# Kernel tuning notes

Measured on AMD Instinct MI355X. Metric: run time of the kernel, lower is better.

Reference implementation:

```python
import jax, jax.numpy as jnp
import numpy as np

RADIUS = 8
NUM = 200
EPS = 1e-8


def _conv2d(x, k, pad_mode):
    # x: [B,1,H,W], k: [kh,kw]; same-size conv with given numpy-style padding mode
    ph, pw = k.shape[0] // 2, k.shape[1] // 2
    xp = jnp.pad(x, ((0, 0), (0, 0), (ph, ph), (pw, pw)), mode=pad_mode)
    return jax.lax.conv_general_dilated(
        xp, k[None, None], (1, 1), 'VALID',
        dimension_numbers=('NCHW', 'OIHW', 'NCHW'))


def _gauss_kernel7():
    xs = np.arange(7, dtype=np.float32) - 3.0
    g = np.exp(-0.5 * xs ** 2)
    g /= g.sum()
    return jnp.asarray(np.outer(g, g))


def get_corners(imgs):
    B, _, H, W = imgs.shape
    # kornia rgb_to_grayscale
    gray = 0.299 * imgs[:, 0:1] + 0.587 * imgs[:, 1:2] + 0.114 * imgs[:, 2:3]
    # kornia CornerGFTT: sobel gradients (normalized), gaussian-smoothed structure tensor, min eigenvalue
    sob = jnp.array([[-1., 0., 1.], [-2., 0., 2.], [-1., 0., 1.]], jnp.float32) / 8.0
    dx = _conv2d(gray, sob, 'edge')
    dy = _conv2d(gray, sob.T, 'edge')
    g = _gauss_kernel7()
    dx2 = _conv2d(dx * dx, g, 'reflect')
    dy2 = _conv2d(dy * dy, g, 'reflect')
    dxy = _conv2d(dx * dy, g, 'reflect')
    tr = dx2 + dy2
    det = dx2 * dy2 - dxy * dxy
    resp = 0.5 * (tr - jnp.sqrt(jnp.abs(tr * tr - 4.0 * det)))  # GFTT score (min eigval)
    # kornia nms2d with 5x5 window: keep local maxima
    mp = jax.lax.reduce_window(resp, -jnp.inf, jax.lax.max,
                               (1, 1, 5, 5), (1, 1, 1, 1),
                               [(0, 0), (0, 0), (2, 2), (2, 2)])
    resp = jnp.where(resp == mp, resp, 0.0)
    # unfold/mask/fold with kernel=stride=RADIUS == per non-overlapping 8x8 block:
    # keep elements equal to the block max and > 0
    r = RADIUS
    blk = resp.reshape(B, 1, H // r, r, W // r, r)
    bmax = blk.max(axis=(3, 5), keepdims=True)
    blk = jnp.where((blk > 0) & (blk == bmax), blk, 0.0)
    corners = blk.reshape(B, H * W)
    # top-200 scatter then binarize
    vals, idx = jax.lax.top_k(corners, NUM)
    out = jnp.zeros_like(corners).at[jnp.arange(B)[:, None], idx].set(vals)
    return (out > 0).astype(imgs.dtype).reshape(B, 1, H, W)


def setup_inputs() -> dict:
    key = jax.random.key(0)
    k1, k2, k3, k4 = jax.random.split(key, 4)
    B, N, D, H, W = 16, 2048, 256, 384, 384
    return {
        'descriptors': jax.random.normal(k1, (B, N, D), jnp.float32),
        'scores': jax.random.uniform(k2, (B, N), jnp.float32),
        'scores_dense': jax.random.normal(k3, (B, 1, H, W), jnp.float32),
        'imgs': jax.random.uniform(k4, (B, 3, H, W), jnp.float32),
    }


def reference(descriptors, scores, scores_dense, imgs):
    corners = get_corners(imgs)
    # all-pairs cosine similarity within each batch: pcos[b,i,j]
    norms = jnp.linalg.norm(descriptors, axis=-1)  # [B,N]
    dots = jnp.einsum('bnd,bmd->bnm', descriptors, descriptors)
    pcos = dots / jnp.maximum(norms[:, :, None] * norms[:, None, :], EPS)
    # BCEWithLogitsLoss(scores_dense, corners), mean reduction
    bce = jnp.mean(jnp.logaddexp(0.0, scores_dense) - scores_dense * corners)
    return bce + jnp.mean(jax.nn.relu(pcos))
```

## Files before the change

kernel.cpp:

```cpp
#include <hip/hip_runtime.h>

#define H 384
#define W 384
#define HWSZ (H * W)
#define NB 16
#define ND 2048
#define DD 256

#define OFF_RESP  256
#define OFF_CVAL  9437440
#define OFF_CPOS  9584896
#define OFF_DESCB 9732352
#define OFF_INV   26509568
#define OFF_PSOFT 26640640
#define OFF_PGEMM 26643200
#define OFF_PCORN 26652160

__device__ __forceinline__ int clampi(int v) { return v < 0 ? 0 : (v > 383 ? 383 : v); }
__device__ __forceinline__ int refl(int v) { return v < 0 ? -v : (v >= 384 ? 766 - v : v); }

__device__ __forceinline__ unsigned f2e4m3(float x) {
  float a = fabsf(x);
  unsigned s = (__float_as_uint(x) >> 31) << 7;
  if (a >= 448.f) return s | 0x7E;
  if (a < 0.015625f) {
    int m = (int)rintf(a * 512.f);
    return s | (unsigned)m;
  }
  unsigned u = __float_as_uint(a);
  u += 0x7FFFF + ((u >> 20) & 1);
  unsigned e = (u >> 23) - 120;
  unsigned m = (u >> 20) & 7;
  return s | (e << 3) | m;
}

typedef float f32x4 __attribute__((ext_vector_type(4)));

__device__ __forceinline__ void load_lds16(const void* g, void* l) {
  __builtin_amdgcn_global_load_lds((const __attribute__((address_space(1))) void*)g,
                                   (__attribute__((address_space(3))) void*)l, 16, 0, 0);
}

__global__ __launch_bounds__(256) void stage1_kernel(const float* __restrict__ imgs,
                                                     float* __restrict__ resp,
                                                     const float* __restrict__ desc,
                                                     unsigned char* __restrict__ descF8,
                                                     float* __restrict__ invn,
                                                     const float4* __restrict__ sd4,
                                                     float* __restrict__ psoft) {
  __shared__ float gl[40][41];
  __shared__ float p0[38][39], p1[38][39], p2[38][39];
  __shared__ float t0[38][33], t1[38][33], t2[38][33];
  __shared__ float r4s[4];

  if (blockIdx.x >= 10496) {
    int sb = blockIdx.x - 10496;
    float s = 0.f;
    int base = sb * 256 + threadIdx.x;
#pragma unroll
    for (int it = 0; it < 4; it++) {
      float4 v = sd4[base + it * 147456];
      s += fmaxf(v.x, 0.f) + log1pf(expf(-fabsf(v.x))) +
           fmaxf(v.y, 0.f) + log1pf(expf(-fabsf(v.y))) +
           fmaxf(v.z, 0.f) + log1pf(expf(-fabsf(v.z))) +
           fmaxf(v.w, 0.f) + log1pf(expf(-fabsf(v.w)));
    }
    for (int off = 32; off; off >>= 1) s += __shfl_down(s, off, 64);
    if ((threadIdx.x & 63) == 0) r4s[threadIdx.x >> 6] = s;
    __syncthreads();
    if (threadIdx.x == 0) psoft[sb] = r4s[0] + r4s[1] + r4s[2] + r4s[3];
    return;
  }

  if (blockIdx.x >= 2304) {
    int wave = threadIdx.x >> 6, lane = threadIdx.x & 63;
    int row = (blockIdx.x - 2304) * 4 + wave;
    const float4* src = (const float4*)(desc + (size_t)row * DD);
    float4 v = src[lane];
    unsigned pk = f2e4m3(v.x) | (f2e4m3(v.y) << 8) | (f2e4m3(v.z) << 16) | (f2e4m3(v.w) << 24);
    ((unsigned*)(descF8 + (size_t)row * DD))[lane] = pk;
    float ss = v.x * v.x + v.y * v.y + v.z * v.z + v.w * v.w;
    for (int off = 32; off; off >>= 1) ss += __shfl_down(ss, off, 64);
    if (lane == 0) invn[row] = 1.f / fmaxf(sqrtf(ss), 1e-4f);
    return;
  }

  const float GW[7] = {0.0044330482f, 0.0540055826f, 0.2420362294f, 0.3990502160f,
                       0.2420362294f, 0.0540055826f, 0.0044330482f};
  int bid = blockIdx.x;
  int b = bid / 144;
  int t = bid % 144;
  int Y0 = (t / 12) * 32, X0 = (t % 12) * 32;
  const float* ib = imgs + (size_t)b * 3 * HWSZ;

  for (int i = threadIdx.x; i < 1600; i += 256) {
    int r = i / 40, c = i % 40;
    int gy = clampi(Y0 - 4 + r), gx = clampi(X0 - 4 + c);
    const float* p = ib + gy * W + gx;
    gl[r][c] = 0.299f * p[0] + 0.587f * p[HWSZ] + 0.114f * p[2 * HWSZ];
  }
  __syncthreads();

  bool interior = (X0 >= 32 && X0 <= 320 && Y0 >= 32 && Y0 <= 320);

  if (interior) {
    for (int g = threadIdx.x; g < 380; g += 256) {
      int r = g % 38, c0 = (g / 38) * 4;
      float w0[6], w1[6], w2[6];
#pragma unroll
      for (int dc = 0; dc < 6; dc++) {
        int cc = c0 + dc; if (cc > 39) cc = 39;
        w0[dc] = gl[r][cc]; w1[dc] = gl[r + 1][cc]; w2[dc] = gl[r + 2][cc];
      }
#pragma unroll
      for (int k = 0; k < 4; k++) {
        int cc = c0 + k;
        if (cc < 38) {
          float a = w0[k], bb = w0[k + 1], cv = w0[k + 2];
          float d = w1[k], e = w1[k + 2];
          float f = w2[k], gg = w2[k + 1], h = w2[k + 2];
          float dx = 0.125f * ((cv - a) + 2.f * (e - d) + (h - f));
          float dy = 0.125f * ((f - a) + 2.f * (gg - bb) + (h - cv));
          p0[r][cc] = dx * dx;
          p1[r][cc] = dy * dy;
          p2[r][cc] = dx * dy;
        }
      }
    }
    __syncthreads();
    for (int g = threadIdx.x; g < 304; g += 256) {
      int r = g >> 3, c0 = (g & 7) * 4;
      float a0[10], a1[10], a2[10];
#pragma unroll
      for (int dc = 0; dc < 10; dc++) {
        a0[dc] = p0[r][c0 + dc]; a1[dc] = p1[r][c0 + dc]; a2[dc] = p2[r][c0 + dc];
      }
#pragma unroll
      for (int k = 0; k < 4; k++) {
        float s0 = 0.f, s1 = 0.f, s2 = 0.f;
#pragma unroll
        for (int j = 0; j < 7; j++) {
          s0 += GW[j] * a0[k + j];
          s1 += GW[j] * a1[k + j];
          s2 += GW[j] * a2[k + j];
        }
        t0[r][c0 + k] = s0; t1[r][c0 + k] = s1; t2[r][c0 + k] = s2;
      }
    }
    __syncthreads();
    {
      int rg = (threadIdx.x >> 5) * 4, c = threadIdx.x & 31;
      float a0[10], a1[10], a2[10];
#pragma unroll
      for (int dr = 0; dr < 10; dr++) {
        a0[dr] = t0[rg + dr][c]; a1[dr] = t1[rg + dr][c]; a2[dr] = t2[rg + dr][c];
      }
#pragma unroll
      for (int k = 0; k < 4; k++) {
        float s0 = 0.f, s1 = 0.f, s2 = 0.f;
#pragma unroll
        for (int j = 0; j < 7; j++) {
          s0 += GW[j] * a0[k + j];
          s1 += GW[j] * a1[k + j];
          s2 += GW[j] * a2[k + j];
        }
        float tr = s0 + s1;
        float det = s0 * s1 - s2 * s2;
        float disc = tr * tr - 4.f * det;
        float rv = 0.5f * (tr - sqrtf(fabsf(disc)));
        resp[(size_t)b * HWSZ + (Y0 + rg + k) * W + (X0 + c)] = rv;
      }
    }
    return;
  }

  for (int i = threadIdx.x; i < 1444; i += 256) {
    int r = i / 38, c = i % 38;
    int py = refl(Y0 - 3 + r), px = refl(X0 - 3 + c);
    int ym = clampi(py - 1) - (Y0 - 4), y0 = py - (Y0 - 4), yp = clampi(py + 1) - (Y0 - 4);
    int xm = clampi(px - 1) - (X0 - 4), x0 = px - (X0 - 4), xp = clampi(px + 1) - (X0 - 4);
    float a = gl[ym][xm], bb = gl[ym][x0], cc = gl[ym][xp];
    float d = gl[y0][xm], e = gl[y0][xp];
    float f = gl[yp][xm], g = gl[yp][x0], h = gl[yp][xp];
    float dx = 0.125f * ((cc - a) + 2.f * (e - d) + (h - f));
    float dy = 0.125f * ((f - a) + 2.f * (g - bb) + (h - cc));
    p0[r][c] = dx * dx;
    p1[r][c] = dy * dy;
    p2[r][c] = dx * dy;
  }
  __syncthreads();

  for (int i = threadIdx.x; i < 1216; i += 256) {
    int r = i / 32, c = i % 32;
    float s0 = 0.f, s1 = 0.f, s2 = 0.f;
#pragma unroll
    for (int j = 0; j < 7; j++) {
      s0 += GW[j] * p0[r][c + j];
      s1 += GW[j] * p1[r][c + j];
      s2 += GW[j] * p2[r][c + j];
    }
    t0[r][c] = s0; t1[r][c] = s1; t2[r][c] = s2;
  }
  __syncthreads();

  for (int i = threadIdx.x; i < 1024; i += 256) {
    int r = i / 32, c = i % 32;
    float s0 = 0.f, s1 = 0.f, s2 = 0.f;
#pragma unroll
    for (int j = 0; j < 7; j++) {
      s0 += GW[j] * t0[r + j][c];
      s1 += GW[j] * t1[r + j][c];
      s2 += GW[j] * t2[r + j][c];
    }
    float tr = s0 + s1;
    float det = s0 * s1 - s2 * s2;
    float disc = tr * tr - 4.f * det;
    float rv = 0.5f * (tr - sqrtf(fabsf(disc)));
    resp[(size_t)b * HWSZ + (Y0 + r) * W + (X0 + c)] = rv;
  }
}

__global__ __launch_bounds__(256) void stage2_kernel(const unsigned char* __restrict__ descF8,
                                                     const float* __restrict__ invn,
                                                     float* __restrict__ pgemm,
                                                     const float* __restrict__ resp,
                                                     float* __restrict__ cval,
                                                     unsigned* __restrict__ cpos) {
  extern __shared__ char smem2[];

  if (blockIdx.x >= 2176) {
    float (*rl)[69] = (float(*)[69])smem2;
    float (*nl)[65] = (float(*)[65])(smem2 + 68 * 69 * 4);
    int bid = blockIdx.x - 2176;
    int b = bid / 36;
    int t = bid % 36;
    int Y0 = (t / 6) * 64, X0 = (t % 6) * 64;
    const float* rb = resp + (size_t)b * HWSZ;

    for (int i = threadIdx.x; i < 68 * 68; i += 256) {
      int r = i / 68, c = i % 68;
      int gy = Y0 - 2 + r, gx = X0 - 2 + c;
      float v = -INFINITY;
      if (gy >= 0 && gy < H && gx >= 0 && gx < W) v = rb[gy * W + gx];
      rl[r][c] = v;
    }
    __syncthreads();

    for (int i = threadIdx.x; i < 4096; i += 256) {
      int r = i / 64, c = i % 64;
      float m = -INFINITY;
#pragma unroll
      for (int dr = 0; dr < 5; dr++)
#pragma unroll
        for (int dc = 0; dc < 5; dc++) m = fmaxf(m, rl[r + dr][c + dc]);
      float v = rl[r + 2][c + 2];
      nl[r][c] = (v == m) ? v : 0.f;
    }
    __syncthreads();

    if (threadIdx.x < 64) {
      int bi = threadIdx.x / 8, bj = threadIdx.x % 8;
      float bv = 0.f;
      unsigned bp = 0;
      for (int rr = 0; rr < 8; rr++)
        for (int cc = 0; cc < 8; cc++) {
          float v = nl[bi * 8 + rr][bj * 8 + cc];
          if (v > bv) { bv = v; bp = (unsigned)((Y0 + bi * 8 + rr) * W + (X0 + bj * 8 + cc)); }
        }
      int ci = b * 2304 + (Y0 / 8 + bi) * 48 + (X0 / 8 + bj);
      cval[ci] = bv;
      cpos[ci] = bp;
    }
    return;
  }

  char* lA = smem2;
  char* lB = smem2 + 16384;
  float* r4 = (float*)(smem2 + 32768);

  int bx = blockIdx.x;
  int batch = bx / 136;
  int rem = bx % 136;
  int ti = 0, rowlen = 16;
  while (rem >= rowlen) { rem -= rowlen; rowlen--; ti++; }
  int tj = ti + rem;

  const unsigned char* Ab = descF8 + (size_t)batch * ND * DD;
  const float* inv = invn + batch * ND;
  int I0 = ti * 128, J0 = tj * 128;

  int tid = threadIdx.x;
  int wave = tid >> 6, lane = tid & 63;
  int rm = lane & 15, kq = lane >> 4;
  int wr = wave >> 1, wc = wave & 1;
  int lrow = lane >> 3;
  int lcolb = ((lane & 7) ^ lrow) << 4;
  int cx = rm & 7;

  f32x4 accf[4][4];
#pragma unroll
  for (int m = 0; m < 4; m++)
#pragma unroll
    for (int n = 0; n < 4; n++) accf[m][n] = (f32x4){0.f, 0.f, 0.f, 0.f};

  for (int k0 = 0; k0 < DD; k0 += 128) {
#pragma unroll
    for (int q = 0; q < 4; q++) {
      int chunk = wave * 4 + q;
      load_lds16(Ab + (size_t)(I0 + chunk * 8 + lrow) * DD + k0 + lcolb, lA + chunk * 1024);
      load_lds16(Ab + (size_t)(J0 + chunk * 8 + lrow) * DD + k0 + lcolb, lB + chunk * 1024);
    }
    __syncthreads();
#pragma unroll
    for (int kk = 0; kk < 128; kk += 32) {
      long af[4], bfr[4];
      int koff = kk + kq * 8;
      int pcol = ((((koff >> 4) ^ cx) << 4) | (koff & 8));
#pragma unroll
      for (int m = 0; m < 4; m++)
        af[m] = *reinterpret_cast<const long*>(lA + (wr * 64 + m * 16 + rm) * 128 + pcol);
#pragma unroll
      for (int n = 0; n < 4; n++)
        bfr[n] = *reinterpret_cast<const long*>(lB + (wc * 64 + n * 16 + rm) * 128 + pcol);
#pragma unroll
      for (int m = 0; m < 4; m++)
#pragma unroll
        for (int n = 0; n < 4; n++)
          accf[m][n] = __builtin_amdgcn_mfma_f32_16x16x32_fp8_fp8(af[m], bfr[n], accf[m][n], 0, 0, 0);
    }
    __syncthreads();
  }

  float wgt = (ti == tj) ? 1.f : 2.f;
  float invC[4];
#pragma unroll
  for (int n = 0; n < 4; n++) invC[n] = inv[J0 + wc * 64 + n * 16 + rm];
  float psum = 0.f;
#pragma unroll
  for (int m = 0; m < 4; m++) {
#pragma unroll
    for (int r = 0; r < 4; r++) {
      float invR = inv[I0 + wr * 64 + m * 16 + kq * 4 + r];
#pragma unroll
      for (int n = 0; n < 4; n++) psum += fmaxf(accf[m][n][r] * invR * invC[n], 0.f);
    }
  }
  psum *= wgt;
  for (int off = 32; off; off >>= 1) psum += __shfl_down(psum, off, 64);
  if (lane == 0) r4[wave] = psum;
  __syncthreads();
  if (tid == 0) pgemm[bx] = r4[0] + r4[1] + r4[2] + r4[3];
}

__global__ __launch_bounds__(256) void topk_kernel(const float* __restrict__ cval,
                                                   const unsigned* __restrict__ cpos,
                                                   const float* __restrict__ sd,
                                                   float* __restrict__ pcorn) {
  __shared__ int hist[256];
  __shared__ int pick[2];
  __shared__ unsigned eqpos[256];
  __shared__ int eqcnt;
  __shared__ float rf[4];
  __shared__ int ri[4];

  int b = blockIdx.x;
  int t = threadIdx.x;
  int lane = t & 63;

  unsigned bits[9], pos[9];
#pragma unroll
  for (int q = 0; q < 9; q++) {
    int i = t + q * 256;
    unsigned vb = 0, p = 0;
    if (i < 2304) {
      float v = cval[b * 2304 + i];
      if (v > 0.f) { vb = __float_as_uint(v); p = cpos[b * 2304 + i]; }
    }
    bits[q] = vb; pos[q] = p;
  }

  int P = 0;
#pragma unroll
  for (int q = 0; q < 9; q++) P += (bits[q] != 0u);
  for (int off = 32; off; off >>= 1) P += __shfl_down(P, off, 64);
  if (lane == 0) ri[t >> 6] = P;
  __syncthreads();
  int Ptot = ri[0] + ri[1] + ri[2] + ri[3];
  if (Ptot == 0) { if (t == 0) pcorn[b] = 0.f; return; }
  int K = Ptot < 200 ? Ptot : 200;

  unsigned prefix = 0;
  int krem = K;
  for (int shift = 24; shift >= 0; shift -= 8) {
    hist[t] = 0;
    __syncthreads();
#pragma unroll
    for (int q = 0; q < 9; q++) {
      if (bits[q] != 0u &&
          (shift == 24 || (bits[q] >> (shift + 8)) == (prefix >> (shift + 8))))
        atomicAdd(&hist[(bits[q] >> shift) & 0xFF], 1);
    }
    __syncthreads();
    if (t < 64) {
      int h0 = hist[4 * t], h1 = hist[4 * t + 1], h2 = hist[4 * t + 2], h3 = hist[4 * t + 3];
      int tot = h0 + h1 + h2 + h3;
      int acc = tot;
      for (int d = 1; d < 64; d <<= 1) {
        int o = __shfl_down(acc, d, 64);
        if (t + d < 64) acc += o;
      }
      int excl = acc - tot;
      int G3 = excl, G2 = excl + h3, G1 = excl + h3 + h2, G0 = excl + h3 + h2 + h1;
      if (G0 < krem && G0 + h0 >= krem) { pick[0] = 4 * t;     pick[1] = G0; }
      if (G1 < krem && G1 + h1 >= krem) { pick[0] = 4 * t + 1; pick[1] = G1; }
      if (G2 < krem && G2 + h2 >= krem) { pick[0] = 4 * t + 2; pick[1] = G2; }
      if (G3 < krem && G3 + h3 >= krem) { pick[0] = 4 * t + 3; pick[1] = G3; }
    }
    __syncthreads();
    prefix |= ((unsigned)pick[0]) << shift;
    krem -= pick[1];
    __syncthreads();
  }

  if (t == 0) eqcnt = 0;
  __syncthreads();
  float s = 0.f;
#pragma unroll
  for (int q = 0; q < 9; q++) {
    if (bits[q] > prefix) s += sd[(size_t)b * HWSZ + pos[q]];
    else if (bits[q] != 0u && bits[q] == prefix) {
      int idx = atomicAdd(&eqcnt, 1);
      if (idx < 256) eqpos[idx] = pos[q];
    }
  }
  __syncthreads();
  int m = eqcnt;
  if (m <= krem) {
    if (t < m) s += sd[(size_t)b * HWSZ + eqpos[t]];
  } else {
    int mm = m < 256 ? m : 256;
    if (t < mm) {
      unsigned p = eqpos[t];
      int rank = 0;
      for (int u = 0; u < mm; u++) rank += (eqpos[u] < p);
      if (rank < krem) s += sd[(size_t)b * HWSZ + p];
    }
  }
  for (int off = 32; off; off >>= 1) s += __shfl_down(s, off, 64);
  if (lane == 0) rf[t >> 6] = s;
  __syncthreads();
  if (t == 0) pcorn[b] = rf[0] + rf[1] + rf[2] + rf[3];
}

__global__ __launch_bounds__(256) void finalize_kernel(const float* __restrict__ psoft,
                                                       const float* __restrict__ pcorn,
                                                       const float* __restrict__ pgemm,
                                                       float* __restrict__ out) {
  __shared__ float r4[4];
  float bce = 0.f;
  for (int i = threadIdx.x; i < 576; i += 256) bce += psoft[i];
  if (threadIdx.x < 16) bce -= pcorn[threadIdx.x];
  float g = 0.f;
  for (int i = threadIdx.x; i < 2176; i += 256) g += pgemm[i];
  float t = bce * (1.f / 2359296.f) + g * (1.f / 67108864.f);
  for (int off = 32; off; off >>= 1) t += __shfl_down(t, off, 64);
  if ((threadIdx.x & 63) == 0) r4[threadIdx.x >> 6] = t;
  __syncthreads();
  if (threadIdx.x == 0) out[0] = r4[0] + r4[1] + r4[2] + r4[3];
}

extern "C" void kernel_launch(void* const* d_in, const int* in_sizes, int n_in,
                              void* d_out, int out_size, void* d_ws, size_t ws_size,
                              hipStream_t stream) {
  (void)in_sizes; (void)n_in; (void)out_size; (void)ws_size;
  const float* desc = (const float*)d_in[0];
  const float* sd = (const float*)d_in[2];
  const float* imgs = (const float*)d_in[3];
  float* out = (float*)d_out;

  char* w = (char*)d_ws;
  float* resp = (float*)(w + OFF_RESP);
  float* cval = (float*)(w + OFF_CVAL);
  unsigned* cpos = (unsigned*)(w + OFF_CPOS);
  unsigned char* descF8 = (unsigned char*)(w + OFF_DESCB);
  float* invn = (float*)(w + OFF_INV);
  float* psoft = (float*)(w + OFF_PSOFT);
  float* pgemm = (float*)(w + OFF_PGEMM);
  float* pcorn = (float*)(w + OFF_PCORN);

  stage1_kernel<<<11072, 256, 0, stream>>>(imgs, resp, desc, descF8, invn,
                                           (const float4*)sd, psoft);
  stage2_kernel<<<2752, 256, 35456, stream>>>(descF8, invn, pgemm, resp, cval, cpos);
  topk_kernel<<<16, 256, 0, stream>>>(cval, cpos, sd, pcorn);
  finalize_kernel<<<1, 256, 0, stream>>>(psoft, pcorn, pgemm, out);
}
```

Baseline: 177.0 us.

## Alias stage1 LDS buffers, vectorize stencil loads, unify separable blur path

Stage1's shared buffers are repacked into two float4 arrays with 40/36-float row pitches, and the grayscale tile is aliased with the horizontal-blur output, which shrinks LDS per block. The Sobel, horizontal and vertical blur passes now use float4/float2 LDS loads and stores, and boundary tiles share the register-blocked blur path with interior tiles. Launch bounds of 4 blocks per CU are added to both stage1 and stage2 to raise occupancy, at the cost of tighter register limits and possible spills. The padding change also alters the LDS bank-conflict pattern.

```diff
diff --git a/kernel.cpp b/kernel.cpp
--- a/kernel.cpp
+++ b/kernel.cpp
@@ -41,19 +41,25 @@
                                    (__attribute__((address_space(3))) void*)l, 16, 0, 0);
 }
 
-__global__ __launch_bounds__(256) void stage1_kernel(const float* __restrict__ imgs,
-                                                     float* __restrict__ resp,
-                                                     const float* __restrict__ desc,
-                                                     unsigned char* __restrict__ descF8,
-                                                     float* __restrict__ invn,
-                                                     const float4* __restrict__ sd4,
-                                                     float* __restrict__ psoft) {
-  __shared__ float gl[40][41];
-  __shared__ float p0[38][39], p1[38][39], p2[38][39];
-  __shared__ float t0[38][33], t1[38][33], t2[38][33];
-  __shared__ float r4s[4];
+__global__ __launch_bounds__(256, 4) void stage1_kernel(const float* __restrict__ imgs,
+                                                        float* __restrict__ resp,
+                                                        const float* __restrict__ desc,
+                                                        unsigned char* __restrict__ descF8,
+                                                        float* __restrict__ invn,
+                                                        const float4* __restrict__ sd4,
+                                                        float* __restrict__ psoft) {
+  __shared__ float4 pbuf4[1140];
+  __shared__ float4 ubuf4[1026];
+  float* p0 = (float*)pbuf4;
+  float* p1 = p0 + 1520;
+  float* p2 = p0 + 3040;
+  float* glf = (float*)ubuf4;
+  float* t0 = (float*)ubuf4;
+  float* t1 = t0 + 1368;
+  float* t2 = t0 + 2736;
 
   if (blockIdx.x >= 10496) {
+    float* r4s = (float*)pbuf4;
     int sb = blockIdx.x - 10496;
     float s = 0.f;
     int base = sb * 256 + threadIdx.x;
@@ -97,7 +103,7 @@
     int r = i / 40, c = i % 40;
     int gy = clampi(Y0 - 4 + r), gx = clampi(X0 - 4 + c);
     const float* p = ib + gy * W + gx;
-    gl[r][c] = 0.299f * p[0] + 0.587f * p[HWSZ] + 0.114f * p[2 * HWSZ];
+    glf[i] = 0.299f * p[0] + 0.587f * p[HWSZ] + 0.114f * p[2 * HWSZ];
   }
   __syncthreads();
 
@@ -105,13 +111,17 @@
 
   if (interior) {
     for (int g = threadIdx.x; g < 380; g += 256) {
-      int r = g % 38, c0 = (g / 38) * 4;
-      float w0[6], w1[6], w2[6];
-#pragma unroll
-      for (int dc = 0; dc < 6; dc++) {
-        int cc = c0 + dc; if (cc > 39) cc = 39;
-        w0[dc] = gl[r][cc]; w1[dc] = gl[r + 1][cc]; w2[dc] = gl[r + 2][cc];
-      }
+      int r = g / 10, c0 = (g % 10) * 4;
+      const float* row = glf + r * 40 + c0;
+      float4 A0 = *(const float4*)(row);
+      float2 B0 = *(const float2*)(row + 4);
+      float4 A1 = *(const float4*)(row + 40);
+      float2 B1 = *(const float2*)(row + 44);
+      float4 A2 = *(const float4*)(row + 80);
+      float2 B2 = *(const float2*)(row + 84);
+      float w0[6] = {A0.x, A0.y, A0.z, A0.w, B0.x, B0.y};
+      float w1[6] = {A1.x, A1.y, A1.z, A1.w, B1.x, B1.y};
+      float w2[6] = {A2.x, A2.y, A2.z, A2.w, B2.x, B2.y};
 #pragma unroll
       for (int k = 0; k < 4; k++) {
         int cc = c0 + k;
@@ -121,111 +131,133 @@
           float f = w2[k], gg = w2[k + 1], h = w2[k + 2];
           float dx = 0.125f * ((cv - a) + 2.f * (e - d) + (h - f));
           float dy = 0.125f * ((f - a) + 2.f * (gg - bb) + (h - cv));
-          p0[r][cc] = dx * dx;
-          p1[r][cc] = dy * dy;
-          p2[r][cc] = dx * dy;
+          p0[r * 40 + cc] = dx * dx;
+          p1[r * 40 + cc] = dy * dy;
+          p2[r * 40 + cc] = dx * dy;
         }
       }
     }
-    __syncthreads();
-    for (int g = threadIdx.x; g < 304; g += 256) {
-      int r = g >> 3, c0 = (g & 7) * 4;
-      float a0[10], a1[10], a2[10];
-#pragma unroll
-      for (int dc = 0; dc < 10; dc++) {
-        a0[dc] = p0[r][c0 + dc]; a1[dc] = p1[r][c0 + dc]; a2[dc] = p2[r][c0 + dc];
-      }
-#pragma unroll
-      for (int k = 0; k < 4; k++) {
-        float s0 = 0.f, s1 = 0.f, s2 = 0.f;
-#pragma unroll
-        for (int j = 0; j < 7; j++) {
-          s0 += GW[j] * a0[k + j];
-          s1 += GW[j] * a1[k + j];
-          s2 += GW[j] * a2[k + j];
-        }
-        t0[r][c0 + k] = s0; t1[r][c0 + k] = s1; t2[r][c0 + k] = s2;
-      }
-    }
-    __syncthreads();
+  } else {
+    for (int i = threadIdx.x; i < 1444; i += 256) {
+      int r = i / 38, c = i % 38;
+      int py = refl(Y0 - 3 + r), px = refl(X0 - 3 + c);
+      int ym = clampi(py - 1) - (Y0 - 4), y0 = py - (Y0 - 4), yp = clampi(py + 1) - (Y0 - 4);
+      int xm = clampi(px - 1) - (X0 - 4), x0 = px - (X0 - 4), xp = clampi(px + 1) - (X0 - 4);
+      float a = glf[ym * 40 + xm], bb = glf[ym * 40 + x0], cc = glf[ym * 40 + xp];
+      float d = glf[y0 * 40 + xm], e = glf[y0 * 40 + xp];
+      float f = glf[yp * 40 + xm], g = glf[yp * 40 + x0], h = glf[yp * 40 + xp];
+      float dx = 0.125f * ((cc - a) + 2.f * (e - d) + (h - f));
+      float dy = 0.125f * ((f - a) + 2.f * (g - bb) + (h - cc));
+      p0[r * 40 + c] = dx * dx;
+      p1[r * 40 + c] = dy * dy;
+      p2[r * 40 + c] = dx * dy;
+    }
+  }
+  __syncthreads();
+
+  for (int g = threadIdx.x; g < 304; g += 256) {
+    int r = g >> 3, c0 = (g & 7) * 4;
     {
-      int rg = (threadIdx.x >> 5) * 4, c = threadIdx.x & 31;
-      float a0[10], a1[10], a2[10];
-#pragma unroll
-      for (int dr = 0; dr < 10; dr++) {
-        a0[dr] = t0[rg + dr][c]; a1[dr] = t1[rg + dr][c]; a2[dr] = t2[rg + dr][c];
-      }
-#pragma unroll
-      for (int k = 0; k < 4; k++) {
-        float s0 = 0.f, s1 = 0.f, s2 = 0.f;
-#pragma unroll
-        for (int j = 0; j < 7; j++) {
-          s0 += GW[j] * a0[k + j];
-          s1 += GW[j] * a1[k + j];
-          s2 += GW[j] * a2[k + j];
-        }
-        float tr = s0 + s1;
-        float det = s0 * s1 - s2 * s2;
-        float disc = tr * tr - 4.f * det;
-        float rv = 0.5f * (tr - sqrtf(fabsf(disc)));
-        resp[(size_t)b * HWSZ + (Y0 + rg + k) * W + (X0 + c)] = rv;
-      }
-    }
-    return;
-  }
-
-  for (int i = threadIdx.x; i < 1444; i += 256) {
-    int r = i / 38, c = i % 38;
-    int py = refl(Y0 - 3 + r), px = refl(X0 - 3 + c);
-    int ym = clampi(py - 1) - (Y0 - 4), y0 = py - (Y0 - 4), yp = clampi(py + 1) - (Y0 - 4);
-    int xm = clampi(px - 1) - (X0 - 4), x0 = px - (X0 - 4), xp = clampi(px + 1) - (X0 - 4);
-    float a = gl[ym][xm], bb = gl[ym][x0], cc = gl[ym][xp];
-    float d = gl[y0][xm], e = gl[y0][xp];
-    float f = gl[yp][xm], g = gl[yp][x0], h = gl[yp][xp];
-    float dx = 0.125f * ((cc - a) + 2.f * (e - d) + (h - f));
-    float dy = 0.125f * ((f - a) + 2.f * (g - bb) + (h - cc));
-    p0[r][c] = dx * dx;
-    p1[r][c] = dy * dy;
-    p2[r][c] = dx * dy;
-  }
-  __syncthreads();
-
-  for (int i = threadIdx.x; i < 1216; i += 256) {
-    int r = i / 32, c = i % 32;
-    float s0 = 0.f, s1 = 0.f, s2 = 0.f;
-#pragma unroll
-    for (int j = 0; j < 7; j++) {
-      s0 += GW[j] * p0[r][c + j];
-      s1 += GW[j] * p1[r][c + j];
-      s2 += GW[j] * p2[r][c + j];
-    }
-    t0[r][c] = s0; t1[r][c] = s1; t2[r][c] = s2;
-  }
-  __syncthreads();
-
-  for (int i = threadIdx.x; i < 1024; i += 256) {
-    int r = i / 32, c = i % 32;
-    float s0 = 0.f, s1 = 0.f, s2 = 0.f;
-#pragma unroll
-    for (int j = 0; j < 7; j++) {
-      s0 += GW[j] * t0[r + j][c];
-      s1 += GW[j] * t1[r + j][c];
-      s2 += GW[j] * t2[r + j][c];
-    }
-    float tr = s0 + s1;
-    float det = s0 * s1 - s2 * s2;
-    float disc = tr * tr - 4.f * det;
-    float rv = 0.5f * (tr - sqrtf(fabsf(disc)));
-    resp[(size_t)b * HWSZ + (Y0 + r) * W + (X0 + c)] = rv;
-  }
-}
-
-__global__ __launch_bounds__(256) void stage2_kernel(const unsigned char* __restrict__ descF8,
-                                                     const float* __restrict__ invn,
-                                                     float* __restrict__ pgemm,
-                                                     const float* __restrict__ resp,
-                                                     float* __restrict__ cval,
-                                                     unsigned* __restrict__ cpos) {
+      const float* pr = p0 + r * 40 + c0;
+      float4 A = *(const float4*)(pr), B = *(const float4*)(pr + 4), C = *(const float4*)(pr + 8);
+      float w[12] = {A.x, A.y, A.z, A.w, B.x, B.y, B.z, B.w, C.x, C.y, C.z, C.w};
+      float s[4];
+#pragma unroll
+      for (int k = 0; k < 4; k++) {
+        float sv = 0.f;
+#pragma unroll
+        for (int j = 0; j < 7; j++) sv += GW[j] * w[k + j];
+        s[k] = sv;
+      }
+      *(float4*)(t0 + r * 36 + c0) = (float4){s[0], s[1], s[2], s[3]};
+    }
+    {
+      const float* pr = p1 + r * 40 + c0;
+      float4 A = *(const float4*)(pr), B = *(const float4*)(pr + 4), C = *(const float4*)(pr + 8);
+      float w[12] = {A.x, A.y, A.z, A.w, B.x, B.y, B.z, B.w, C.x, C.y, C.z, C.w};
+      float s[4];
+#pragma unroll
+      for (int k = 0; k < 4; k++) {
+        float sv = 0.f;
+#pragma unroll
+        for (int j = 0; j < 7; j++) sv += GW[j] * w[k + j];
+        s[k] = sv;
+      }
+      *(float4*)(t1 + r * 36 + c0) = (float4){s[0], s[1], s[2], s[3]};
+    }
+    {
+      const float* pr = p2 + r * 40 + c0;
+      float4 A = *(const float4*)(pr), B = *(const float4*)(pr + 4), C = *(const float4*)(pr + 8);
+      float w[12] = {A.x, A.y, A.z, A.w, B.x, B.y, B.z, B.w, C.x, C.y, C.z, C.w};
+      float s[4];
+#pragma unroll
+      for (int k = 0; k < 4; k++) {
+        float sv = 0.f;
+#pragma unroll
+        for (int j = 0; j < 7; j++) sv += GW[j] * w[k + j];
+        s[k] = sv;
+      }
+      *(float4*)(t2 + r * 36 + c0) = (float4){s[0], s[1], s[2], s[3]};
+    }
+  }
+  __syncthreads();
+
+  {
+    int r0 = (threadIdx.x >> 5) * 4, c = threadIdx.x & 31;
+    float s0[4], s1[4], s2[4];
+    {
+      float a[10];
+#pragma unroll
+      for (int dr = 0; dr < 10; dr++) a[dr] = t0[(r0 + dr) * 36 + c];
+#pragma unroll
+      for (int k = 0; k < 4; k++) {
+        float sv = 0.f;
+#pragma unroll
+        for (int j = 0; j < 7; j++) sv += GW[j] * a[k + j];
+        s0[k] = sv;
+      }
+    }
+    {
+      float a[10];
+#pragma unroll
+      for (int dr = 0; dr < 10; dr++) a[dr] = t1[(r0 + dr) * 36 + c];
+#pragma unroll
+      for (int k = 0; k < 4; k++) {
+        float sv = 0.f;
+#pragma unroll
+        for (int j = 0; j < 7; j++) sv += GW[j] * a[k + j];
+        s1[k] = sv;
+      }
+    }
+    {
+      float a[10];
+#pragma unroll
+      for (int dr = 0; dr < 10; dr++) a[dr] = t2[(r0 + dr) * 36 + c];
+#pragma unroll
+      for (int k = 0; k < 4; k++) {
+        float sv = 0.f;
+#pragma unroll
+        for (int j = 0; j < 7; j++) sv += GW[j] * a[k + j];
+        s2[k] = sv;
+      }
+    }
+#pragma unroll
+    for (int k = 0; k < 4; k++) {
+      float tr = s0[k] + s1[k];
+      float det = s0[k] * s1[k] - s2[k] * s2[k];
+      float disc = tr * tr - 4.f * det;
+      float rv = 0.5f * (tr - sqrtf(fabsf(disc)));
+      resp[(size_t)b * HWSZ + (Y0 + r0 + k) * W + (X0 + c)] = rv;
+    }
+  }
+}
+
+__global__ __launch_bounds__(256, 4) void stage2_kernel(const unsigned char* __restrict__ descF8,
+                                                        const float* __restrict__ invn,
+                                                        float* __restrict__ pgemm,
+                                                        const float* __restrict__ resp,
+                                                        float* __restrict__ cval,
+                                                        unsigned* __restrict__ cpos) {
   extern __shared__ char smem2[];
 
   if (blockIdx.x >= 2176) {
```

Measured after the change: 174.2 us. Within noise of the previous version (-1.6%).
